# Kernel optimization log

Hardware: AMD Instinct MI355X
Metric: run time of the kernel (lower is better)

The kernel has to match this reference:

```python
import jax, jax.numpy as jnp
import numpy as np

KH, KW = 3, 3
PAD = (1, 1, 1, 1)  # torch F.pad order: (W_left, W_right, H_top, H_bottom)
STRIDE = 1
B, CIN, COUT, H, W = 4, 32, 32, 128, 128


def setup_inputs() -> dict:
    key = jax.random.key(0)
    k1, k2, k3, k4 = jax.random.split(key, 4)
    f = jax.random.normal(k1, (B, CIN, H, W), jnp.float32)
    # orientation field components (cos/sin of a random angle field)
    theta = jax.random.uniform(k2, (B, CIN, H, W), jnp.float32, 0.0, 2.0 * np.pi)
    r0 = jnp.cos(theta)
    r1 = jnp.sin(theta)
    # learned conv weight (nn.Conv2d default uniform init, no bias)
    fan_in = CIN * KH * KW
    bound = 1.0 / np.sqrt(fan_in)
    w = jax.random.uniform(k3, (COUT, CIN, KH, KW), jnp.float32, -bound, bound)
    # frozen wr: (randn * pi * 100) / a with a = 100  ->  randn * pi
    wr = jax.random.normal(k4, (COUT, CIN, KH, KW), jnp.float32) * np.pi
    return {"f": f, "r0": r0, "r1": r1, "w": w, "wr": wr}


def _rot90(w):
    # torch: w.permute(0,1,2,4,3).flip([4]) on the (kh,kw) dims
    return jnp.flip(jnp.swapaxes(w, -1, -2), -1)


def _conv_single(f, r0, r1, w, wr):
    # f, r0, r1: (B, Cin, Hp, Wp);  w, wr: (Cout, Cin, KH, KW)
    Hp, Wp = f.shape[2], f.shape[3]
    he = Hp - PAD[0] - PAD[1]
    we = Wp - PAD[2] - PAD[3]
    s = STRIDE
    out = None
    for i in range(KH):
        for j in range(KW):
            fw = f[:, :, i:i + he:s, j:j + we:s]    # (B, Cin, h, w)
            r0w = r0[:, :, i:i + he:s, j:j + we:s]
            r1w = r1[:, :, i:i + he:s, j:j + we:s]
            c = jnp.cos(wr[:, :, i, j])[None, :, :, None, None]   # (1, Cout, Cin, 1, 1)
            sn = jnp.sin(wr[:, :, i, j])[None, :, :, None, None]
            # lambda_theta: relu of orientation-projected field, (B, Cout, Cin, h, w)
            lam = jax.nn.relu(c * r0w[:, None] + sn * r1w[:, None])
            term = jnp.einsum('bchw,oc,bochw->bohw', fw, w[:, :, i, j], lam)
            out = term if out is None else out + term
    return out  # (B, Cout, h, w)


def _forward(f, r0, r1, w, wr):
    pl, pr, pt, pb = PAD
    pad = ((0, 0), (0, 0), (pt, pb), (pl, pr))
    fp = jnp.pad(f, pad)
    r0p = jnp.pad(r0, pad)
    r1p = jnp.pad(r1, pad)
    orient = jnp.arange(4, dtype=f.dtype) * jnp.asarray(np.pi / 2, f.dtype)
    outs = []
    wk = w
    for o in range(4):
        if o > 0:
            wk = _rot90(wk)
        outs.append(_conv_single(fp, r0p, r1p, wk, wr + orient[o]))
    stacked = jnp.stack(outs, axis=2)              # (B, Cout, 4, h, w)
    idx = jnp.argmax(stacked, axis=2)              # (B, Cout, h, w)
    out = jnp.take_along_axis(stacked, idx[:, :, None], axis=2)[:, :, 0]
    out_r = orient[idx]                            # winning orientation angle
    return out, jnp.cos(out_r), jnp.sin(out_r)


def reference(f, r0, r1, w, wr):
    return _forward(f, r0, r1, w, wr)
```

## Files before the change

kernel.cpp:

```cpp
#include <hip/hip_runtime.h>


typedef float v2f __attribute__((ext_vector_type(2)));

#define B_    4
#define CIN_  32
#define COUT_ 32
#define H_    128
#define W_    128
#define HW_   (H_ * W_)
#define OUTSZ_ (B_ * COUT_ * H_ * W_)

__global__ __launch_bounds__(256)
void build_wtab(const float* __restrict__ w, const float* __restrict__ wr,
                float* __restrict__ tab)
{
    int idx = blockIdx.x * 256 + threadIdx.x;
    if (idx >= CIN_ * 9 * COUT_) return;
    int oc  = idx & 31;
    int t2  = idx >> 5;
    int tap = t2 % 9;
    int cc  = t2 / 9;
    int i = tap / 3, j = tap - i * 3;
    int base = (oc * CIN_ + cc) * 9;
    float w0 = w[base + i * 3 + j];
    float w1 = w[base + (2 - j) * 3 + i];
    float w2 = w[base + (2 - i) * 3 + (2 - j)];
    float w3 = w[base + j * 3 + (2 - i)];
    float S, C;
    sincosf(wr[base + i * 3 + j], &S, &C);
    float* dst = tab + (size_t)idx * 8;
    dst[0] = C;  dst[1] = S;
    dst[2] = w0; dst[3] = w1;
    dst[4] = w2; dst[5] = w3;
    dst[6] = 0.0f; dst[7] = 0.0f;
}

#define NC_    8
#define NG_    (CIN_ / NC_)
#define ROWF_  68
#define CLSTR_ (3 * ROWF_)
#define USED_  (NC_ * CLSTR_)
#define PLANE_ 1636

__global__ __launch_bounds__(512, 4)
void orient_conv_kernel(const float* __restrict__ f,
                        const float* __restrict__ r0,
                        const float* __restrict__ r1,
                        const float* __restrict__ tab,
                        float* __restrict__ out)
{
    __shared__ float sm[3 * PLANE_];

    const int tid   = threadIdx.x;
    const int oc    = tid & 31;
    const int pxg   = tid >> 5;
    const int p     = pxg << 1;
    const int bid   = blockIdx.x;
    const int b     = bid >> 8;
    const int rem   = bid & 255;
    const int h     = rem >> 1;
    const int wbase = (rem & 1) << 6;

    int      goff[4], sidx[4];
    unsigned msk[4];
#pragma unroll
    for (int k = 0; k < 4; ++k) {
        int s = tid + (k << 9);
        if (s < USED_) {
            int cl  = s / CLSTR_;
            int r2  = s - cl * CLSTR_;
            int row = r2 / ROWF_;
            int q2  = r2 - row * ROWF_;
            int col = (q2 >> 1) + ((q2 & 1) << 5);
            int gh = h + row - 1;
            int gw = wbase + col - 1;
            bool ok = ((unsigned)gh < (unsigned)H_) & ((unsigned)gw < (unsigned)W_);
            goff[k] = ok ? (cl * HW_ + gh * W_ + gw) : 0;
            msk[k]  = ok ? 0xFFFFFFFFu : 0u;
            sidx[k] = s;
        } else { goff[k] = 0; msk[k] = 0u; sidx[k] = USED_; }
    }
    const bool have3 = (tid + 1536) < USED_;
    const int chanBase = b * (CIN_ * HW_);

    v2f acc[2][4];
#pragma unroll
    for (int q = 0; q < 2; ++q)
#pragma unroll
        for (int o = 0; o < 4; ++o) acc[q][o] = (v2f)(0.0f);

    float tF[4], tA[4], tB[4];
    {
        const float* fb = f  + chanBase;
        const float* ab = r0 + chanBase;
        const float* bb = r1 + chanBase;
#pragma unroll
        for (int k = 0; k < 3; ++k) {
            tF[k] = fb[goff[k]]; tA[k] = ab[goff[k]]; tB[k] = bb[goff[k]];
        }
        if (have3) { tF[3] = fb[goff[3]]; tA[3] = ab[goff[3]]; tB[3] = bb[goff[3]]; }
    }

#pragma unroll 1
    for (int g = 0; g < NG_; ++g) {
        __syncthreads();
#pragma unroll
        for (int k = 0; k < 3; ++k) {
            sm[             sidx[k]] = __uint_as_float(__float_as_uint(tF[k]) & msk[k]);
            sm[PLANE_     + sidx[k]] = __uint_as_float(__float_as_uint(tA[k]) & msk[k]);
            sm[2 * PLANE_ + sidx[k]] = __uint_as_float(__float_as_uint(tB[k]) & msk[k]);
        }
        if (have3) {
            sm[             sidx[3]] = __uint_as_float(__float_as_uint(tF[3]) & msk[3]);
            sm[PLANE_     + sidx[3]] = __uint_as_float(__float_as_uint(tA[3]) & msk[3]);
            sm[2 * PLANE_ + sidx[3]] = __uint_as_float(__float_as_uint(tB[3]) & msk[3]);
        }
        __syncthreads();

        if (g + 1 < NG_) {
            const int gb = chanBase + (g + 1) * (NC_ * HW_);
            const float* fb = f  + gb;
            const float* ab = r0 + gb;
            const float* bb = r1 + gb;
#pragma unroll
            for (int k = 0; k < 3; ++k) {
                tF[k] = fb[goff[k]]; tA[k] = ab[goff[k]]; tB[k] = bb[goff[k]];
            }
            if (have3) { tF[3] = fb[goff[3]]; tA[3] = ab[goff[3]]; tB[3] = bb[goff[3]]; }
        }

#pragma unroll 1
        for (int cl = 0; cl < NC_; ++cl) {
            const int cc = g * NC_ + cl;
            const float* wb0 = tab + (size_t)(((cc * 9 + 2) << 5) | oc) * 8;
            const float* wb1 = wb0 + 4 * 256;
#pragma unroll
            for (int i = 0; i < 3; ++i) {
                const int bi = cl * CLSTR_ + i * ROWF_ + (p << 1);
                float4 fA = *reinterpret_cast<const float4*>(&sm[bi]);
                float4 fB = *reinterpret_cast<const float4*>(&sm[bi + 4]);
                float4 aA = *reinterpret_cast<const float4*>(&sm[PLANE_ + bi]);
                float4 aB = *reinterpret_cast<const float4*>(&sm[PLANE_ + bi + 4]);
                float4 bA = *reinterpret_cast<const float4*>(&sm[2 * PLANE_ + bi]);
                float4 bB = *reinterpret_cast<const float4*>(&sm[2 * PLANE_ + bi + 4]);
                v2f fP[4]  = {{fA.x, fA.y}, {fA.z, fA.w}, {fB.x, fB.y}, {fB.z, fB.w}};
                v2f aP[4]  = {{aA.x, aA.y}, {aA.z, aA.w}, {aB.x, aB.y}, {aB.z, aB.w}};
                v2f bP[4]  = {{bA.x, bA.y}, {bA.z, bA.w}, {bB.x, bB.y}, {bB.z, bB.w}};
#pragma unroll
                for (int j = 0; j < 3; ++j) {
                    const int tap = i * 3 + j;
                    const float* wp = (tap < 5) ? (wb0 + (tap - 2) * 256)
                                                : (wb1 + (tap - 6) * 256);
                    float4 W4 = *reinterpret_cast<const float4*>(wp);
                    float2 W2 = *reinterpret_cast<const float2*>(wp + 4);
                    v2f C2  = {W4.x, W4.x};
                    v2f S2  = {W4.y, W4.y};
                    v2f w02 = {W4.z, W4.z};
                    v2f w12 = {W4.w, W4.w};
                    v2f w22 = {W2.x, W2.x};
                    v2f w32 = {W2.y, W2.y};
#pragma unroll
                    for (int q = 0; q < 2; ++q) {
                        v2f fv  = fP[q + j];
                        v2f r0v = aP[q + j];
                        v2f r1v = bP[q + j];
                        v2f m1 = S2 * r1v;
                        v2f u  = __builtin_elementwise_fma(C2, r0v, m1);
                        v2f m2 = S2 * r0v;
                        v2f vv = __builtin_elementwise_fma(C2, r1v, -m2);
                        v2f g0 = __builtin_elementwise_max(u,  (v2f)(0.0f));
                        v2f g1 = __builtin_elementwise_max(vv, (v2f)(0.0f));
                        v2f t0 = fv * g0;
                        v2f t1 = fv * g1;
                        v2f t2 = __builtin_elementwise_fma(fv, -u,  t0);
                        v2f t3 = __builtin_elementwise_fma(fv, -vv, t1);
                        acc[q][0] = __builtin_elementwise_fma(t0, w02, acc[q][0]);
                        acc[q][1] = __builtin_elementwise_fma(t1, w12, acc[q][1]);
                        acc[q][2] = __builtin_elementwise_fma(t2, w22, acc[q][2]);
                        acc[q][3] = __builtin_elementwise_fma(t3, w32, acc[q][3]);
                    }
                }
            }
        }
    }

    const float cosv[4] = {1.0f, -4.37113883e-08f, -1.0f, 1.19248806e-08f};
    const float sinv[4] = {0.0f, 1.0f, -8.74227766e-08f, -1.0f};
#pragma unroll
    for (int q = 0; q < 2; ++q) {
#pragma unroll
        for (int k = 0; k < 2; ++k) {
            int wcol = wbase + p + q + (k << 5);
            float a0 = acc[q][0][k], a1 = acc[q][1][k];
            float a2 = acc[q][2][k], a3 = acc[q][3][k];
            float best = a0; int bi = 0;
            if (a1 > best) { best = a1; bi = 1; }
            if (a2 > best) { best = a2; bi = 2; }
            if (a3 > best) { best = a3; bi = 3; }
            size_t o = ((size_t)(b * COUT_ + oc) * H_ + h) * W_ + wcol;
            out[o]              = best;
            out[o + OUTSZ_]     = cosv[bi];
            out[o + 2 * OUTSZ_] = sinv[bi];
        }
    }
}

extern "C" void kernel_launch(void* const* d_in, const int* in_sizes, int n_in,
                              void* d_out, int out_size, void* d_ws, size_t ws_size,
                              hipStream_t stream)
{
    const float* f  = (const float*)d_in[0];
    const float* r0 = (const float*)d_in[1];
    const float* r1 = (const float*)d_in[2];
    const float* w  = (const float*)d_in[3];
    const float* wr = (const float*)d_in[4];
    float* out = (float*)d_out;
    float* tab = (float*)d_ws;

    build_wtab<<<dim3(36), dim3(256), 0, stream>>>(w, wr, tab);
    orient_conv_kernel<<<dim3(B_ * H_ * 2), dim3(512), 0, stream>>>(
        f, r0, r1, tab, out);
}
```

Baseline: 290.3 us.

## Software-pipeline weight-table loads one kernel row ahead with double-buffered registers

Weight-table loads move out of the inner tap loop into a ping-pong register buffer (WA/WB). Each step prefetches the next row's three taps while computing the current row, using a running offset clamped at the end of the table. A sched_group_barrier groups the six loads together, and launch bounds drop from 4 to 3 waves per SIMD to make room for the extra registers. The goal is to hide global or L2 latency on the weight loads, at the cost of lower occupancy.

```diff
diff --git a/kernel.cpp b/kernel.cpp
--- a/kernel.cpp
+++ b/kernel.cpp
@@ -43,7 +43,72 @@
 #define USED_  (NC_ * CLSTR_)
 #define PLANE_ 1636
 
-__global__ __launch_bounds__(512, 4)
+struct WRow { float4 a0, a1, a2; float2 b0, b1, b2; };
+
+#define LOAD_WROW(Wd) do {                                                  \
+    const float* _wp = wanchor + soff;                                      \
+    (Wd).a0 = *reinterpret_cast<const float4*>(_wp - 256);                  \
+    (Wd).b0 = *reinterpret_cast<const float2*>(_wp - 252);                  \
+    (Wd).a1 = *reinterpret_cast<const float4*>(_wp);                        \
+    (Wd).b1 = *reinterpret_cast<const float2*>(_wp + 4);                    \
+    (Wd).a2 = *reinterpret_cast<const float4*>(_wp + 256);                  \
+    (Wd).b2 = *reinterpret_cast<const float2*>(_wp + 260);                  \
+    soff += 768;                                                            \
+    soff = (soff < 72960) ? soff : 72960;    \
+    __builtin_amdgcn_sched_group_barrier(0x020, 6, 0);    \
+} while (0)
+
+#define CORE_TAP(W4, W2, JJ) do {                                           \
+    v2f _C2  = {(W4).x, (W4).x};                                            \
+    v2f _S2  = {(W4).y, (W4).y};                                            \
+    v2f _w0  = {(W4).z, (W4).z};                                            \
+    v2f _w1  = {(W4).w, (W4).w};                                            \
+    v2f _w2  = {(W2).x, (W2).x};                                            \
+    v2f _w3  = {(W2).y, (W2).y};                                            \
+    _Pragma("unroll")                                                       \
+    for (int _q = 0; _q < 2; ++_q) {                                        \
+        v2f _f  = _fP[_q + (JJ)];                                           \
+        v2f _r0 = _aP[_q + (JJ)];                                           \
+        v2f _r1 = _bP[_q + (JJ)];                                           \
+        v2f _m1 = _S2 * _r1;                                                \
+        v2f _u  = __builtin_elementwise_fma(_C2, _r0, _m1);                 \
+        v2f _m2 = _S2 * _r0;                                                \
+        v2f _vv = __builtin_elementwise_fma(_C2, _r1, -_m2);                \
+        v2f _g0 = __builtin_elementwise_max(_u,  (v2f)(0.0f));              \
+        v2f _g1 = __builtin_elementwise_max(_vv, (v2f)(0.0f));              \
+        v2f _t0 = _f * _g0;                                                 \
+        v2f _t1 = _f * _g1;                                                 \
+        v2f _t2 = __builtin_elementwise_fma(_f, -_u,  _t0);                 \
+        v2f _t3 = __builtin_elementwise_fma(_f, -_vv, _t1);                 \
+        acc[_q][0] = __builtin_elementwise_fma(_t0, _w0, acc[_q][0]);       \
+        acc[_q][1] = __builtin_elementwise_fma(_t1, _w1, acc[_q][1]);       \
+        acc[_q][2] = __builtin_elementwise_fma(_t2, _w2, acc[_q][2]);       \
+        acc[_q][3] = __builtin_elementwise_fma(_t3, _w3, acc[_q][3]);       \
+    }                                                                       \
+} while (0)
+
+#define COMPUTE_ROW(Wr, CL, II) do {                                        \
+    const int _bi = (CL) * CLSTR_ + (II) * ROWF_ + (p << 1);                \
+    float4 _fA = *reinterpret_cast<const float4*>(&sm[_bi]);                \
+    float4 _fB = *reinterpret_cast<const float4*>(&sm[_bi + 4]);            \
+    float4 _aA = *reinterpret_cast<const float4*>(&sm[PLANE_ + _bi]);       \
+    float4 _aB = *reinterpret_cast<const float4*>(&sm[PLANE_ + _bi + 4]);   \
+    float4 _bA = *reinterpret_cast<const float4*>(&sm[2 * PLANE_ + _bi]);   \
+    float4 _bB = *reinterpret_cast<const float4*>(&sm[2 * PLANE_ + _bi + 4]);\
+    v2f _fP[4] = {{_fA.x,_fA.y},{_fA.z,_fA.w},{_fB.x,_fB.y},{_fB.z,_fB.w}}; \
+    v2f _aP[4] = {{_aA.x,_aA.y},{_aA.z,_aA.w},{_aB.x,_aB.y},{_aB.z,_aB.w}}; \
+    v2f _bP[4] = {{_bA.x,_bA.y},{_bA.z,_bA.w},{_bB.x,_bB.y},{_bB.z,_bB.w}}; \
+    CORE_TAP((Wr).a0, (Wr).b0, 0);                                          \
+    CORE_TAP((Wr).a1, (Wr).b1, 1);                                          \
+    CORE_TAP((Wr).a2, (Wr).b2, 2);                                          \
+} while (0)
+
+#define STEP(WLD, WUSE, CL, II) do {                                        \
+    LOAD_WROW(WLD);                                                         \
+    COMPUTE_ROW(WUSE, CL, II);                                              \
+} while (0)
+
+__global__ __launch_bounds__(512, 3)
 void orient_conv_kernel(const float* __restrict__ f,
                         const float* __restrict__ r0,
                         const float* __restrict__ r1,
@@ -90,6 +155,11 @@
 #pragma unroll
         for (int o = 0; o < 4; ++o) acc[q][o] = (v2f)(0.0f);
 
+    const float* wanchor = tab + (size_t)((1 << 5) | oc) * 8;
+    int soff = 0;
+    WRow WA, WB;
+    LOAD_WROW(WA);
+
     float tF[4], tA[4], tB[4];
     {
         const float* fb = f  + chanBase;
@@ -131,57 +201,13 @@
         }
 
 #pragma unroll 1
-        for (int cl = 0; cl < NC_; ++cl) {
-            const int cc = g * NC_ + cl;
-            const float* wb0 = tab + (size_t)(((cc * 9 + 2) << 5) | oc) * 8;
-            const float* wb1 = wb0 + 4 * 256;
-#pragma unroll
-            for (int i = 0; i < 3; ++i) {
-                const int bi = cl * CLSTR_ + i * ROWF_ + (p << 1);
-                float4 fA = *reinterpret_cast<const float4*>(&sm[bi]);
-                float4 fB = *reinterpret_cast<const float4*>(&sm[bi + 4]);
-                float4 aA = *reinterpret_cast<const float4*>(&sm[PLANE_ + bi]);
-                float4 aB = *reinterpret_cast<const float4*>(&sm[PLANE_ + bi + 4]);
-                float4 bA = *reinterpret_cast<const float4*>(&sm[2 * PLANE_ + bi]);
-                float4 bB = *reinterpret_cast<const float4*>(&sm[2 * PLANE_ + bi + 4]);
-                v2f fP[4]  = {{fA.x, fA.y}, {fA.z, fA.w}, {fB.x, fB.y}, {fB.z, fB.w}};
-                v2f aP[4]  = {{aA.x, aA.y}, {aA.z, aA.w}, {aB.x, aB.y}, {aB.z, aB.w}};
-                v2f bP[4]  = {{bA.x, bA.y}, {bA.z, bA.w}, {bB.x, bB.y}, {bB.z, bB.w}};
-#pragma unroll
-                for (int j = 0; j < 3; ++j) {
-                    const int tap = i * 3 + j;
-                    const float* wp = (tap < 5) ? (wb0 + (tap - 2) * 256)
-                                                : (wb1 + (tap - 6) * 256);
-                    float4 W4 = *reinterpret_cast<const float4*>(wp);
-                    float2 W2 = *reinterpret_cast<const float2*>(wp + 4);
-                    v2f C2  = {W4.x, W4.x};
-                    v2f S2  = {W4.y, W4.y};
-                    v2f w02 = {W4.z, W4.z};
-                    v2f w12 = {W4.w, W4.w};
-                    v2f w22 = {W2.x, W2.x};
-                    v2f w32 = {W2.y, W2.y};
-#pragma unroll
-                    for (int q = 0; q < 2; ++q) {
-                        v2f fv  = fP[q + j];
-                        v2f r0v = aP[q + j];
-                        v2f r1v = bP[q + j];
-                        v2f m1 = S2 * r1v;
-                        v2f u  = __builtin_elementwise_fma(C2, r0v, m1);
-                        v2f m2 = S2 * r0v;
-                        v2f vv = __builtin_elementwise_fma(C2, r1v, -m2);
-                        v2f g0 = __builtin_elementwise_max(u,  (v2f)(0.0f));
-                        v2f g1 = __builtin_elementwise_max(vv, (v2f)(0.0f));
-                        v2f t0 = fv * g0;
-                        v2f t1 = fv * g1;
-                        v2f t2 = __builtin_elementwise_fma(fv, -u,  t0);
-                        v2f t3 = __builtin_elementwise_fma(fv, -vv, t1);
-                        acc[q][0] = __builtin_elementwise_fma(t0, w02, acc[q][0]);
-                        acc[q][1] = __builtin_elementwise_fma(t1, w12, acc[q][1]);
-                        acc[q][2] = __builtin_elementwise_fma(t2, w22, acc[q][2]);
-                        acc[q][3] = __builtin_elementwise_fma(t3, w32, acc[q][3]);
-                    }
-                }
-            }
+        for (int cl = 0; cl < NC_; cl += 2) {
+            STEP(WB, WA, cl,     0);
+            STEP(WA, WB, cl,     1);
+            STEP(WB, WA, cl,     2);
+            STEP(WA, WB, cl + 1, 0);
+            STEP(WB, WA, cl + 1, 1);
+            STEP(WA, WB, cl + 1, 2);
         }
     }
 
```

New measurement: 270.3 us. 1.07x faster.
